# Kernel optimization log

Measured on AMD Instinct MI355X. Metric: run time of the kernel, lower is better.

Reference implementation:

```python
import jax, jax.numpy as jnp
import numpy as np
from jax import lax

D_MODEL, D_INNER, D_STATE, D_CONV, DT_RANK = 1024, 2048, 16, 4, 64
B_SZ, L = 2, 2048


def silu(v):
    return v * jax.nn.sigmoid(v)


def setup_inputs() -> dict:
    key = jax.random.key(0)
    ks = jax.random.split(key, 9)
    s = 0.02
    x = jax.random.normal(ks[0], (B_SZ, L, D_MODEL), jnp.float32)
    W_in = jax.random.normal(ks[1], (D_MODEL, 2 * D_INNER), jnp.float32) * s
    conv_w = jax.random.normal(ks[2], (D_INNER, D_CONV), jnp.float32) * 0.1  # depthwise kernel
    conv_b = jax.random.normal(ks[3], (D_INNER,), jnp.float32) * 0.01
    W_xproj = jax.random.normal(ks[4], (D_INNER, DT_RANK + 2 * D_STATE), jnp.float32) * s
    W_dt = jax.random.normal(ks[5], (DT_RANK, D_INNER), jnp.float32) * s
    b_dt = jax.random.normal(ks[6], (D_INNER,), jnp.float32) * 0.01
    A_log = jnp.log(jnp.tile(jnp.arange(1, D_STATE + 1, dtype=jnp.float32), (D_INNER, 1)))
    D = jnp.ones((D_INNER,), jnp.float32)
    W_out = jax.random.normal(ks[7], (D_INNER, D_MODEL), jnp.float32) * s
    return dict(x=x, W_in=W_in, conv_w=conv_w, conv_b=conv_b, W_xproj=W_xproj,
                W_dt=W_dt, b_dt=b_dt, A_log=A_log, D=D, W_out=W_out)


def reference(x, W_in, conv_w, conv_b, W_xproj, W_dt, b_dt, A_log, D, W_out):
    # in_proj, split into conv path u and gate res
    xr = x @ W_in                                  # (B, L, 2*d_inner)
    u, res = jnp.split(xr, 2, axis=-1)
    # causal depthwise conv1d (left-pad d_conv-1), then SiLU
    uc = jnp.swapaxes(u, 1, 2)                     # (B, C, L)
    uc = lax.conv_general_dilated(
        uc, conv_w[:, None, :], window_strides=(1,),
        padding=[(D_CONV - 1, 0)], feature_group_count=D_INNER,
        dimension_numbers=('NCH', 'OIH', 'NCH'))
    uc = uc + conv_b[None, :, None]
    u = silu(jnp.swapaxes(uc, 1, 2))               # (B, L, d_inner)
    # S6 projections
    x_dbl = u @ W_xproj                            # (B, L, dt_rank + 2*N)
    dt_low = x_dbl[..., :DT_RANK]
    Bm = x_dbl[..., DT_RANK:DT_RANK + D_STATE]     # (B, L, N)
    Cm = x_dbl[..., DT_RANK + D_STATE:]            # (B, L, N)
    dt = jax.nn.softplus(dt_low @ W_dt + b_dt)     # (B, L, d_inner)
    A = -jnp.exp(A_log)                            # (d_inner, N)
    # selective scan over time
    def step(h, inp):
        dt_t, B_t, C_t, u_t = inp                  # (B,d), (B,N), (B,N), (B,d)
        dA = jnp.exp(dt_t[:, :, None] * A)         # (B, d, N)
        dBu = dt_t[:, :, None] * B_t[:, None, :] * u_t[:, :, None]
        h = dA * h + dBu
        y = jnp.sum(h * C_t[:, None, :], axis=-1)  # (B, d)
        return h, y
    h0 = jnp.zeros((B_SZ, D_INNER, D_STATE), u.dtype)
    xs = (jnp.swapaxes(dt, 0, 1), jnp.swapaxes(Bm, 0, 1),
          jnp.swapaxes(Cm, 0, 1), jnp.swapaxes(u, 0, 1))
    _, ys = lax.scan(step, h0, xs)
    y = jnp.swapaxes(ys, 0, 1) + u * D             # (B, L, d_inner)
    # gate and out_proj
    y = y * silu(res)
    return y @ W_out
```

## Files before the change

### kernel.cpp

```cpp
#include <hip/hip_runtime.h>
#include <cstdint>
#include <cstddef>

#define DMODEL 1024
#define DINNER 2048
#define DSTATE 16
#define DCONV  4
#define DTRANK 64
#define BSZ    2
#define SEQL   2048
#define MROWS  (BSZ*SEQL)
#define NCHUNK 32
#define CLEN   (SEQL/NCHUNK)

typedef __bf16 bf16;
typedef bf16  bf16x8 __attribute__((ext_vector_type(8)));
typedef bf16  bf16x4 __attribute__((ext_vector_type(4)));
typedef float floatx4 __attribute__((ext_vector_type(4)));

#define EPILDC 136
#define SLDC   64

__device__ __forceinline__ float fsigmoid(float x){ return 1.f/(1.f+__expf(-x)); }
__device__ __forceinline__ float fsilu(float x){ return x*fsigmoid(x); }

__device__ __forceinline__ void gload_lds16(const void* g, void* l){
  __builtin_amdgcn_global_load_lds((__attribute__((address_space(1))) void*)g,
                                   (__attribute__((address_space(3))) void*)l,
                                   16, 0, 0);
}

__global__ void k_prep(const float* __restrict__ x, bf16* __restrict__ xb,
                       const float* __restrict__ W_in, const float* __restrict__ W_out,
                       const float* __restrict__ W_xproj, const float* __restrict__ W_dt,
                       bf16* __restrict__ WinT, bf16* __restrict__ WoutT,
                       bf16* __restrict__ WxT, bf16* __restrict__ WdtT){
  __shared__ float tile[32][33];
  int b = blockIdx.x;
  if (b < 4096){
    int i = (b*256 + threadIdx.x)*4;
    float4 v = *(const float4*)(x + i);
    bf16x4 o; o[0]=(bf16)v.x; o[1]=(bf16)v.y; o[2]=(bf16)v.z; o[3]=(bf16)v.w;
    *(bf16x4*)(xb + i) = o;
    return;
  }
  b -= 4096;
  const float* in; bf16* out; int R, C, outR, nbx;
  if      (b < 4096)            { in=W_in;    out=WinT;  R=1024; C=4096; outR=4096; nbx=128; }
  else if (b < 4096+2048)       { b-=4096;    in=W_out;  out=WoutT; R=2048; C=1024; outR=1024; nbx=32; }
  else if (b < 4096+2048+256)   { b-=6144;    in=W_xproj;out=WxT;  R=2048; C=96;   outR=128;  nbx=4; }
  else                          { b-=6400;    in=W_dt;   out=WdtT; R=64;   C=2048; outR=2048; nbx=64; }
  int c0 = (b % nbx)*32, r0 = (b / nbx)*32;
  int tx = threadIdx.x & 31, ty = threadIdx.x >> 5;
  #pragma unroll
  for (int ii=0; ii<4; ++ii){
    int r = r0 + ty + ii*8, c = c0 + tx;
    float v = 0.f;
    if (r < R && c < C) v = in[(size_t)r*C + c];
    tile[ty+ii*8][tx] = v;
  }
  __syncthreads();
  #pragma unroll
  for (int ii=0; ii<4; ++ii){
    int orow = c0 + ty + ii*8;
    int ocol = r0 + tx;
    if (orow < outR && ocol < R) out[(size_t)orow*R + ocol] = (bf16)tile[tx][ty+ii*8];
  }
}

__global__ __launch_bounds__(512, 2)
void k_gemm_in256(const bf16* __restrict__ A, const bf16* __restrict__ Bt,
                  bf16* __restrict__ C1, bf16* __restrict__ C2){
  extern __shared__ __align__(16) bf16 lds[];
  const int tid  = threadIdx.x;
  const int lane = tid & 63;
  const int wave = tid >> 6;
  const int quad = lane >> 4;
  const int mrow = lane & 15;
  const int wr = wave >> 2, wc = wave & 3;
  const int bm = blockIdx.y * 256, bn = blockIdx.x * 256;

  floatx4 acc[8][4];
  #pragma unroll
  for (int i=0;i<8;++i)
    #pragma unroll
    for (int j=0;j<4;++j) acc[i][j] = (floatx4){0.f,0.f,0.f,0.f};

  auto stage_tile = [&](int kt, int p){
    #pragma unroll
    for (int mat=0; mat<2; ++mat){
      const bf16* G = mat ? Bt : A;
      const int gb  = mat ? bn : bm;
      bf16* dst = lds + mat*32768 + p*16384 + tid*8;
      #pragma unroll
      for (int l=0; l<4; ++l){
        int L  = l*512 + tid;
        int rl = L >> 3;
        int cg = (L & 7) ^ (rl & 7);
        gload_lds16(G + (size_t)(gb + rl)*1024 + kt*64 + cg*8, dst + l*4096);
      }
    }
  };

  stage_tile(0, 0);

  for (int kt = 0; kt < 16; ++kt){
    const int p = kt & 1;
    if (kt < 15){
      stage_tile(kt+1, p^1);
      asm volatile("s_waitcnt vmcnt(8)" ::: "memory");
    } else {
      asm volatile("s_waitcnt vmcnt(0)" ::: "memory");
    }
    asm volatile("s_barrier" ::: "memory");
    const bf16* bA = lds + p*16384;
    const bf16* bB = lds + 32768 + p*16384;
    #pragma unroll
    for (int kk=0; kk<2; ++kk){
      bf16x8 bfr[4];
      #pragma unroll
      for (int j=0;j<4;++j){
        int r = wc*64 + j*16 + mrow;
        bfr[j] = *(const bf16x8*)(bB + r*64 + ((((kk<<2)|quad) ^ (r&7))*8));
      }
      #pragma unroll
      for (int mh=0; mh<2; ++mh){
        bf16x8 af[4];
        #pragma unroll
        for (int i=0;i<4;++i){
          int r = wr*128 + mh*64 + i*16 + mrow;
          af[i] = *(const bf16x8*)(bA + r*64 + ((((kk<<2)|quad) ^ (r&7))*8));
        }
        __builtin_amdgcn_s_setprio(1);
        #pragma unroll
        for (int i=0;i<4;++i)
          #pragma unroll
          for (int j=0;j<4;++j)
            acc[mh*4+i][j] = __builtin_amdgcn_mfma_f32_16x16x32_bf16(af[i], bfr[j], acc[mh*4+i][j], 0,0,0);
        __builtin_amdgcn_s_setprio(0);
      }
    }
    asm volatile("s_barrier" ::: "memory");
  }

  const bool isres = (bn >= DINNER);
  bf16* dst0 = isres ? (C2 + (bn - DINNER)) : (C1 + bn);
  #pragma unroll
  for (int h=0; h<2; ++h){
    asm volatile("s_barrier" ::: "memory");
    if (wr == h){
      #pragma unroll
      for (int a=0;a<8;++a){
        #pragma unroll
        for (int r=0;r<4;++r){
          int lrow = (a>>2)*64 + (a&3)*16 + quad*4 + r;
          #pragma unroll
          for (int j=0;j<4;++j){
            int lcol = wc*64 + j*16 + mrow;
            float v = acc[a][j][r];
            lds[lrow*264 + lcol] = (bf16)(isres ? fsilu(v) : v);
          }
        }
      }
    }
    asm volatile("s_barrier" ::: "memory");
    {
      int rr = tid >> 2, seg = (tid & 3)*64;
      bf16* gy = dst0 + (size_t)(bm + h*128 + rr)*DINNER + seg;
      #pragma unroll
      for (int i=0;i<8;++i)
        *(bf16x8*)(gy + i*8) = *(const bf16x8*)(lds + rr*264 + seg + i*8);
    }
  }
}

template<int EPI>
__global__ __launch_bounds__(256)
void k_gemm_bt(const bf16* __restrict__ A, const bf16* __restrict__ Bt,
               int M, int N, int K,
               float* __restrict__ C0, bf16* __restrict__ C1, bf16* __restrict__ C2,
               const float* __restrict__ bias){
  __shared__ bf16 lds[17408];
  const int tid  = threadIdx.x;
  const int lane = tid & 63;
  const int wave = tid >> 6;
  const int quad = lane >> 4;
  const int mrow = lane & 15;
  const int wr = wave >> 1, wc = wave & 1;
  const int bm = blockIdx.y * 128, bn = blockIdx.x * 128;
  const int Ks   = K / gridDim.z;
  const int kbeg = blockIdx.z * Ks;

  floatx4 acc[4][4];
  #pragma unroll
  for (int i=0;i<4;++i)
    #pragma unroll
    for (int j=0;j<4;++j) acc[i][j] = (floatx4){0.f,0.f,0.f,0.f};

  const int ar0 = tid >> 2;
  const int kc  = ((tid & 3) ^ ((ar0 >> 1) & 3)) * 8;
  const bf16* Ag0 = A  + (size_t)(bm + ar0)      * K + kc;
  const bf16* Ag1 = A  + (size_t)(bm + ar0 + 64) * K + kc;
  const bf16* Bg0 = Bt + (size_t)(bn + ar0)      * K + kc;
  const bf16* Bg1 = Bt + (size_t)(bn + ar0 + 64) * K + kc;
  const int ksl = (mrow >> 1) & 3;

  auto stage = [&](int k0, int p){
    bf16* bA = lds + p*4096;
    bf16* bB = lds + 8192 + p*4096;
    gload_lds16(Ag0 + k0, bA + (size_t)tid*8);
    gload_lds16(Ag1 + k0, bA + (size_t)(256+tid)*8);
    gload_lds16(Bg0 + k0, bB + (size_t)tid*8);
    gload_lds16(Bg1 + k0, bB + (size_t)(256+tid)*8);
  };

  stage(kbeg, 0);
  int p = 0;
  for (int k0 = kbeg; k0 < kbeg + Ks; k0 += 32){
    __syncthreads();
    if (k0 + 32 < kbeg + Ks) stage(k0 + 32, p ^ 1);
    const bf16* bA = lds + p*4096;
    const bf16* bB = lds + 8192 + p*4096;
    bf16x8 af[4], bfr[4];
    #pragma unroll
    for (int i=0;i<4;++i)
      af[i] = *(const bf16x8*)(bA + (wr*64 + i*16 + mrow)*32 + (quad ^ ksl)*8);
    #pragma unroll
    for (int j=0;j<4;++j)
      bfr[j] = *(const bf16x8*)(bB + (wc*64 + j*16 + mrow)*32 + (quad ^ ksl)*8);
    #pragma unroll
    for (int i=0;i<4;++i)
      #pragma unroll
      for (int j=0;j<4;++j)
        acc[i][j] = __builtin_amdgcn_mfma_f32_16x16x32_bf16(af[i], bfr[j], acc[i][j], 0,0,0);
    p ^= 1;
  }

  if (EPI == 0){
    float* Cz = C0 + (size_t)blockIdx.z * M * N;
    #pragma unroll
    for (int i=0;i<4;++i){
      #pragma unroll
      for (int r=0;r<4;++r){
        int row = bm + wr*64 + i*16 + quad*4 + r;
        #pragma unroll
        for (int j=0;j<4;++j){
          int col = bn + wc*64 + j*16 + mrow;
          Cz[(size_t)row*N + col] = acc[i][j][r];
        }
      }
    }
  } else {
    __syncthreads();
    const bool isres = (bn >= DINNER);
    #pragma unroll
    for (int i=0;i<4;++i)
      #pragma unroll
      for (int r=0;r<4;++r){
        int lrow = wr*64 + i*16 + quad*4 + r;
        #pragma unroll
        for (int j=0;j<4;++j){
          int lcol = wc*64 + j*16 + mrow;
          float v = acc[i][j][r];
          lds[lrow*EPILDC + lcol] = (bf16)(isres ? fsilu(v) : v);
        }
      }
    __syncthreads();
    bf16* dst = isres ? (C2 + (bn - DINNER)) : (C1 + bn);
    const int rr = tid >> 1, hh = (tid & 1)*64;
    #pragma unroll
    for (int i=0;i<8;++i)
      *(bf16x8*)(dst + (size_t)(bm + rr)*DINNER + hh + i*8) =
        *(const bf16x8*)(lds + rr*EPILDC + hh + i*8);
  }
}

__global__ void k_xdbl_reduce(const float* __restrict__ part, float* __restrict__ xdbl,
                              bf16* __restrict__ dtlowb){
  int t = blockIdx.x*blockDim.x + threadIdx.x;
  int i4 = t*4;
  floatx4 acc = (floatx4){0.f,0.f,0.f,0.f};
  #pragma unroll
  for (int z=0; z<8; ++z)
    acc += *(const floatx4*)(part + (size_t)z*MROWS*128 + i4);
  *(floatx4*)(xdbl + i4) = acc;
  int r = i4 >> 7, c = i4 & 127;
  if (c < DTRANK){
    bf16x4 o; o[0]=(bf16)acc[0]; o[1]=(bf16)acc[1]; o[2]=(bf16)acc[2]; o[3]=(bf16)acc[3];
    *(bf16x4*)(dtlowb + (size_t)r*DTRANK + c) = o;
  }
}

__global__ void k_out_reduce(const float* __restrict__ part, float* __restrict__ out){
  int i4 = (blockIdx.x*blockDim.x + threadIdx.x)*4;
  floatx4 a = *(const floatx4*)(part + i4);
  floatx4 b = *(const floatx4*)(part + (size_t)MROWS*DMODEL + i4);
  *(floatx4*)(out + i4) = a + b;
}

__global__ void k_conv_silu(const bf16* __restrict__ u_pre,
                            const float* __restrict__ conv_w,
                            const float* __restrict__ conv_b,
                            bf16* __restrict__ ub){
  int t   = blockIdx.x*blockDim.x + threadIdx.x;
  int d4  = (t & (DINNER/4-1))*4;
  int row = t >> 9;
  int l   = row & (SEQL-1);
  float4 cb = *(const float4*)(conv_b + d4);
  float acc[4] = {cb.x, cb.y, cb.z, cb.w};
  float4 w0 = *(const float4*)(conv_w + (d4+0)*4);
  float4 w1 = *(const float4*)(conv_w + (d4+1)*4);
  float4 w2 = *(const float4*)(conv_w + (d4+2)*4);
  float4 w3 = *(const float4*)(conv_w + (d4+3)*4);
  float wk[4][4] = {{w0.x,w0.y,w0.z,w0.w},{w1.x,w1.y,w1.z,w1.w},
                    {w2.x,w2.y,w2.z,w2.w},{w3.x,w3.y,w3.z,w3.w}};
  #pragma unroll
  for (int k=0;k<4;++k){
    int lk = l + k - 3;
    if (lk >= 0){
      bf16x4 uv = *(const bf16x4*)(u_pre + (size_t)(row + k - 3)*DINNER + d4);
      #pragma unroll
      for (int j=0;j<4;++j) acc[j] += (float)uv[j] * wk[j][k];
    }
  }
  bf16x4 o;
  #pragma unroll
  for (int j=0;j<4;++j) o[j] = (bf16)fsilu(acc[j]);
  *(bf16x4*)(ub + (size_t)row*DINNER + d4) = o;
}

__device__ __forceinline__ void dt_tile_stage(const bf16* __restrict__ dtlow,
                                              const bf16* __restrict__ WdtT,
                                              int base_row, int d0, int tid,
                                              bf16* sdt, bf16* swdt){
  int r  = tid >> 2;
  int c2 = (tid & 3)*2, sw = r & 7;
  const bf16* gA = dtlow + (size_t)(base_row + r)*DTRANK + c2*8;
  const bf16* gB = WdtT  + (size_t)(d0 + r)*DTRANK + c2*8;
  *(bf16x8*)(sdt  + r*64 + ((c2  )^sw)*8) = *(const bf16x8*)(gA);
  *(bf16x8*)(sdt  + r*64 + ((c2+1)^sw)*8) = *(const bf16x8*)(gA + 8);
  *(bf16x8*)(swdt + r*64 + ((c2  )^sw)*8) = *(const bf16x8*)(gB);
  *(bf16x8*)(swdt + r*64 + ((c2+1)^sw)*8) = *(const bf16x8*)(gB + 8);
}

__device__ __forceinline__ void dt_tile_compute(const float* __restrict__ b_dt,
                                                int d0, int tid,
                                                bf16* sdt, const bf16* swdt){
  int wave = tid >> 6, lane = tid & 63;
  int quad = lane >> 4, mrow = lane & 15;
  int arow = wave*16 + mrow;
  bf16x8 af0 = *(const bf16x8*)(sdt + arow*64 + ((quad    ) ^ (arow&7))*8);
  bf16x8 af1 = *(const bf16x8*)(sdt + arow*64 + ((quad + 4) ^ (arow&7))*8);
  #pragma unroll
  for (int dj=0; dj<4; ++dj){
    int brow = dj*16 + mrow;
    bf16x8 bf0 = *(const bf16x8*)(swdt + brow*64 + ((quad    ) ^ (brow&7))*8);
    bf16x8 bf1 = *(const bf16x8*)(swdt + brow*64 + ((quad + 4) ^ (brow&7))*8);
    floatx4 a = (floatx4){0.f,0.f,0.f,0.f};
    a = __builtin_amdgcn_mfma_f32_16x16x32_bf16(af0, bf0, a, 0,0,0);
    a = __builtin_amdgcn_mfma_f32_16x16x32_bf16(af1, bf1, a, 0,0,0);
    float bias = b_dt[d0 + dj*16 + mrow];
    #pragma unroll
    for (int rr=0; rr<4; ++rr){
      float z = a[rr] + bias;
      float sp = fmaxf(z, 0.f) + __logf(1.f + __expf(-fabsf(z)));
      sdt[(wave*16 + quad*4 + rr)*64 + dj*16 + mrow] = (bf16)sp;
    }
  }
}

__global__ void k_scan_phase1(const bf16* __restrict__ dtlow, const bf16* __restrict__ WdtT,
                              const float* __restrict__ b_dt,
                              const bf16* __restrict__ ub,
                              const float* __restrict__ x_dbl, const float* __restrict__ A_log,
                              float* __restrict__ Pbuf, float* __restrict__ Sbuf){
  __shared__ bf16 sdt[64*64], sub[64*SLDC], swdt[64*64];
  __shared__ float sB[64*16];
  const int tid = threadIdx.x;
  int t  = blockIdx.x*256 + tid;
  int g  = t & 3;
  int d  = (t >> 2) & (DINNER-1);
  int dloc = d & 63, d0 = d & ~63;
  int bc = t >> 13;
  int c  = bc & (NCHUNK-1);
  int b  = bc >> 5;
  int base_row = b*SEQL + c*CLEN;
  {
    int r = tid >> 2, ch = (tid & 3)*16;
    const bf16* gu = ub + (size_t)(base_row + r)*DINNER + d0 + ch;
    *(bf16x8*)(sub + r*SLDC + ch)     = *(const bf16x8*)(gu);
    *(bf16x8*)(sub + r*SLDC + ch + 8) = *(const bf16x8*)(gu + 8);
    int q = tid & 3;
    *(floatx4*)(sB + r*16 + q*4) =
      *(const floatx4*)(x_dbl + (size_t)(base_row + r)*128 + DTRANK + q*4);
    dt_tile_stage(dtlow, WdtT, base_row, d0, tid, sdt, swdt);
  }
  floatx4 alog = *(const floatx4*)(A_log + d*DSTATE + g*4);
  float an[4];
  #pragma unroll
  for (int n=0;n<4;++n) an[n] = -__expf(alog[n]);
  __syncthreads();
  dt_tile_compute(b_dt, d0, tid, sdt, swdt);
  __syncthreads();
  float sumdt = 0.f, S[4] = {0.f,0.f,0.f,0.f};
  #pragma unroll 8
  for (int s=0; s<CLEN; ++s){
    float dtv = (float)sdt[s*SLDC + dloc];
    float du  = dtv * (float)sub[s*SLDC + dloc];
    floatx4 Bv = *(const floatx4*)(sB + s*16 + g*4);
    sumdt += dtv;
    #pragma unroll
    for (int n=0;n<4;++n){
      float e = __expf(dtv*an[n]);
      S[n]  = fmaf(S[n], e, du*Bv[n]);
    }
  }
  size_t ob = ((size_t)bc*DINNER + d)*DSTATE + g*4;
  floatx4 Pv, Sv = {S[0],S[1],S[2],S[3]};
  #pragma unroll
  for (int n=0;n<4;++n) Pv[n] = __expf(an[n]*sumdt);
  *(floatx4*)(Pbuf + ob) = Pv;
  *(floatx4*)(Sbuf + ob) = Sv;
}

__global__ void k_scan_phase2(const float* __restrict__ Pbuf, float* __restrict__ Sbuf){
  int t = blockIdx.x*blockDim.x + threadIdx.x;
  int b   = t >> 15;
  int rem = t & 32767;
  float h = 0.f;
  for (int c=0;c<NCHUNK;++c){
    size_t ix = (size_t)(b*NCHUNK + c)*DINNER*DSTATE + rem;
    float p = Pbuf[ix], s = Sbuf[ix];
    Sbuf[ix] = h;
    h = fmaf(p, h, s);
  }
}

__global__ void k_scan_phase3(const bf16* __restrict__ dtlow, const bf16* __restrict__ WdtT,
                              const float* __restrict__ b_dt,
                              const bf16* __restrict__ ub,
                              const float* __restrict__ x_dbl, const float* __restrict__ A_log,
                              const float* __restrict__ Dvec, const float* __restrict__ Hin,
                              const bf16* __restrict__ resb, bf16* __restrict__ yb){
  __shared__ bf16 sdt[64*64], sub[64*SLDC], srs[64*SLDC], swdt[64*64];
  __shared__ float sBC[64*32];
  bf16* syb = swdt;
  const int tid = threadIdx.x;
  int t  = blockIdx.x*256 + tid;
  int g  = t & 3;
  int d  = (t >> 2) & (DINNER-1);
  int dloc = d & 63, d0 = d & ~63;
  int bc = t >> 13;
  int c  = bc & (NCHUNK-1);
  int b  = bc >> 5;
  int base_row = b*SEQL + c*CLEN;
  {
    int r = tid >> 2, ch = (tid & 3)*16;
    const bf16* gu = ub   + (size_t)(base_row + r)*DINNER + d0 + ch;
    const bf16* gr = resb + (size_t)(base_row + r)*DINNER + d0 + ch;
    *(bf16x8*)(sub + r*SLDC + ch)     = *(const bf16x8*)(gu);
    *(bf16x8*)(sub + r*SLDC + ch + 8) = *(const bf16x8*)(gu + 8);
    *(bf16x8*)(srs + r*SLDC + ch)     = *(const bf16x8*)(gr);
    *(bf16x8*)(srs + r*SLDC + ch + 8) = *(const bf16x8*)(gr + 8);
    int q = tid & 3;
    const float* gx = x_dbl + (size_t)(base_row + r)*128 + DTRANK;
    *(floatx4*)(sBC + r*32 + q*4)      = *(const floatx4*)(gx + q*4);
    *(floatx4*)(sBC + r*32 + 16 + q*4) = *(const floatx4*)(gx + DSTATE + q*4);
    dt_tile_stage(dtlow, WdtT, base_row, d0, tid, sdt, swdt);
  }
  floatx4 alog = *(const floatx4*)(A_log + d*DSTATE + g*4);
  float an[4];
  #pragma unroll
  for (int n=0;n<4;++n) an[n] = -__expf(alog[n]);
  floatx4 h = *(const floatx4*)(Hin + ((size_t)bc*DINNER + d)*DSTATE + g*4);
  float Dd = Dvec[d];
  __syncthreads();
  dt_tile_compute(b_dt, d0, tid, sdt, swdt);
  __syncthreads();
  #pragma unroll 8
  for (int s=0; s<CLEN; ++s){
    float dtv = (float)sdt[s*SLDC + dloc];
    float uv  = (float)sub[s*SLDC + dloc];
    float du  = dtv*uv;
    floatx4 Bv = *(const floatx4*)(sBC + s*32 + g*4);
    floatx4 Cv = *(const floatx4*)(sBC + s*32 + 16 + g*4);
    float y = 0.f;
    #pragma unroll
    for (int n=0;n<4;++n){
      float e = __expf(dtv*an[n]);
      h[n] = fmaf(h[n], e, du*Bv[n]);
      y = fmaf(h[n], Cv[n], y);
    }
    y += __shfl_xor(y, 1);
    y += __shfl_xor(y, 2);
    if (g == 0){
      y = (y + uv*Dd) * (float)srs[s*SLDC + dloc];
      syb[s*64 + dloc] = (bf16)y;
    }
  }
  __syncthreads();
  {
    int r = tid >> 2, ch = (tid & 3)*16;
    bf16* gy = yb + (size_t)(base_row + r)*DINNER + d0 + ch;
    *(bf16x8*)(gy)     = *(const bf16x8*)(syb + r*64 + ch);
    *(bf16x8*)(gy + 8) = *(const bf16x8*)(syb + r*64 + ch + 8);
  }
}

extern "C" void kernel_launch(void* const* d_in, const int* in_sizes, int n_in,
                              void* d_out, int out_size, void* d_ws, size_t ws_size,
                              hipStream_t stream){
  const float* x      = (const float*)d_in[0];
  const float* W_in   = (const float*)d_in[1];
  const float* conv_w = (const float*)d_in[2];
  const float* conv_b = (const float*)d_in[3];
  const float* W_xproj= (const float*)d_in[4];
  const float* W_dt   = (const float*)d_in[5];
  const float* b_dt   = (const float*)d_in[6];
  const float* A_log  = (const float*)d_in[7];
  const float* Dv     = (const float*)d_in[8];
  const float* W_out  = (const float*)d_in[9];
  float* out = (float*)d_out;

  uint8_t* wp = (uint8_t*)d_ws;
  auto alloc = [&](size_t bytes)->void*{ void* p = wp; wp += (bytes + 255) & ~(size_t)255; return p; };
  bf16*  xb     = (bf16*) alloc((size_t)MROWS*DMODEL*2);
  bf16*  WinT   = (bf16*) alloc((size_t)2*DINNER*DMODEL*2);
  bf16*  WoutT  = (bf16*) alloc((size_t)DMODEL*DINNER*2);
  bf16*  WxT    = (bf16*) alloc((size_t)128*DINNER*2);
  bf16*  WdtT   = (bf16*) alloc((size_t)DINNER*DTRANK*2);
  bf16*  updt   = (bf16*) alloc((size_t)MROWS*DINNER*2);
  float* scanPS = (float*)alloc((size_t)2*BSZ*NCHUNK*DSTATE*DINNER*4);
  float* Pbuf   = scanPS;
  float* Sbuf   = scanPS + (size_t)BSZ*NCHUNK*DSTATE*DINNER;
  float* xdbl_part = scanPS;
  float* outpart   = (float*)updt;
  bf16*  resb   = (bf16*) alloc((size_t)MROWS*DINNER*2);
  bf16*  ub     = (bf16*) alloc((size_t)MROWS*DINNER*2);
  float* xdbl   = (float*)alloc((size_t)MROWS*128*4);
  bf16*  dtlowb = (bf16*) alloc((size_t)MROWS*DTRANK*2);
  bf16*  yb     = (bf16*) alloc((size_t)MROWS*DINNER*2);

  static bool lds_attr_set = false;
  if (!lds_attr_set){
    hipFuncSetAttribute((const void*)k_gemm_in256,
                        hipFuncAttributeMaxDynamicSharedMemorySize, 131072);
    lds_attr_set = true;
  }

  k_prep<<<4096 + 4096+2048+256+128, 256, 0, stream>>>(x, xb, W_in, W_out, W_xproj, W_dt,
                                                       WinT, WoutT, WxT, WdtT);

  k_gemm_in256<<<dim3(4096/256, 4096/256), 512, 131072, stream>>>(xb, WinT, updt, resb);
  k_conv_silu<<<MROWS*DINNER/4/256, 256, 0, stream>>>(updt, conv_w, conv_b, ub);
  k_gemm_bt<0><<<dim3(1, 4096/128, 8), 256, 0, stream>>>(ub, WxT, MROWS, 128, DINNER, xdbl_part, nullptr, nullptr, nullptr);
  k_xdbl_reduce<<<(MROWS*128/4)/256, 256, 0, stream>>>(xdbl_part, xdbl, dtlowb);
  k_scan_phase1<<<BSZ*NCHUNK*DINNER*4/256, 256, 0, stream>>>(dtlowb, WdtT, b_dt, ub, xdbl, A_log, Pbuf, Sbuf);
  k_scan_phase2<<<BSZ*DINNER*DSTATE/256, 256, 0, stream>>>(Pbuf, Sbuf);
  k_scan_phase3<<<BSZ*NCHUNK*DINNER*4/256, 256, 0, stream>>>(dtlowb, WdtT, b_dt, ub, xdbl, A_log, Dv, Sbuf, resb, yb);
  k_gemm_bt<0><<<dim3(1024/128, 4096/128, 2), 256, 0, stream>>>(yb, WoutT, MROWS, DMODEL, DINNER, outpart, nullptr, nullptr, nullptr);
  k_out_reduce<<<(MROWS*DMODEL/4)/256, 256, 0, stream>>>(outpart, out);
}
```

Before: 309.8 us.

## Interleave in-proj GEMM loads with MFMA phases; drop split-K on out-proj

The 256x256 in-projection GEMM now issues the next tile's A and B loads separately and interleaves them with four barrier-separated MFMA phases, so global-to-LDS copies overlap compute in finer steps. The out-projection GEMM no longer uses 2-way split-K plus a separate reduce kernel. It writes fp32 output directly through a new LDS-staged epilogue with coalesced vector stores. The trade-off is many more barriers per k-step in the big GEMM, and half as many blocks (256) for the output GEMM.

Measured after the change: 317.5 us. 1.02x slower.

```diff
diff --git a/kernel.cpp b/kernel.cpp
--- a/kernel.cpp
+++ b/kernel.cpp
@@ -86,60 +86,91 @@
     #pragma unroll
     for (int j=0;j<4;++j) acc[i][j] = (floatx4){0.f,0.f,0.f,0.f};
 
-  auto stage_tile = [&](int kt, int p){
-    #pragma unroll
-    for (int mat=0; mat<2; ++mat){
-      const bf16* G = mat ? Bt : A;
-      const int gb  = mat ? bn : bm;
-      bf16* dst = lds + mat*32768 + p*16384 + tid*8;
-      #pragma unroll
-      for (int l=0; l<4; ++l){
-        int L  = l*512 + tid;
-        int rl = L >> 3;
-        int cg = (L & 7) ^ (rl & 7);
-        gload_lds16(G + (size_t)(gb + rl)*1024 + kt*64 + cg*8, dst + l*4096);
-      }
+  auto issue_mat = [&](int kt, int p, int mat){
+    const bf16* G = mat ? Bt : A;
+    const int gb  = mat ? bn : bm;
+    bf16* dst = lds + mat*32768 + p*16384 + tid*8;
+    #pragma unroll
+    for (int l=0; l<4; ++l){
+      int L  = l*512 + tid;
+      int rl = L >> 3;
+      int cg = (L & 7) ^ (rl & 7);
+      gload_lds16(G + (size_t)(gb + rl)*1024 + kt*64 + cg*8, dst + l*4096);
     }
   };
 
-  stage_tile(0, 0);
+  auto read_af = [&](const bf16* bA, int mh, int kk, bf16x8* af){
+    #pragma unroll
+    for (int i=0;i<4;++i){
+      int r = wr*128 + mh*64 + i*16 + mrow;
+      af[i] = *(const bf16x8*)(bA + r*64 + ((((kk<<2)|quad) ^ (r&7))*8));
+    }
+  };
+  auto read_bf = [&](const bf16* bB, int kk, bf16x8* bfr){
+    #pragma unroll
+    for (int j=0;j<4;++j){
+      int r = wc*64 + j*16 + mrow;
+      bfr[j] = *(const bf16x8*)(bB + r*64 + ((((kk<<2)|quad) ^ (r&7))*8));
+    }
+  };
+
+  issue_mat(0,0,0); issue_mat(0,0,1);
 
   for (int kt = 0; kt < 16; ++kt){
     const int p = kt & 1;
+    const bf16* bA = lds + p*16384;
+    const bf16* bB = lds + 32768 + p*16384;
+    bf16x8 af[4], bfr[4];
+
     if (kt < 15){
-      stage_tile(kt+1, p^1);
-      asm volatile("s_waitcnt vmcnt(8)" ::: "memory");
+      issue_mat(kt+1, p^1, 0);
+      asm volatile("s_waitcnt vmcnt(4)" ::: "memory");
     } else {
       asm volatile("s_waitcnt vmcnt(0)" ::: "memory");
     }
     asm volatile("s_barrier" ::: "memory");
-    const bf16* bA = lds + p*16384;
-    const bf16* bB = lds + 32768 + p*16384;
-    #pragma unroll
-    for (int kk=0; kk<2; ++kk){
-      bf16x8 bfr[4];
-      #pragma unroll
-      for (int j=0;j<4;++j){
-        int r = wc*64 + j*16 + mrow;
-        bfr[j] = *(const bf16x8*)(bB + r*64 + ((((kk<<2)|quad) ^ (r&7))*8));
-      }
-      #pragma unroll
-      for (int mh=0; mh<2; ++mh){
-        bf16x8 af[4];
-        #pragma unroll
-        for (int i=0;i<4;++i){
-          int r = wr*128 + mh*64 + i*16 + mrow;
-          af[i] = *(const bf16x8*)(bA + r*64 + ((((kk<<2)|quad) ^ (r&7))*8));
-        }
-        __builtin_amdgcn_s_setprio(1);
-        #pragma unroll
-        for (int i=0;i<4;++i)
-          #pragma unroll
-          for (int j=0;j<4;++j)
-            acc[mh*4+i][j] = __builtin_amdgcn_mfma_f32_16x16x32_bf16(af[i], bfr[j], acc[mh*4+i][j], 0,0,0);
-        __builtin_amdgcn_s_setprio(0);
-      }
-    }
+    read_af(bA, 0, 0, af); read_bf(bB, 0, bfr);
+    __builtin_amdgcn_s_setprio(1);
+    #pragma unroll
+    for (int i=0;i<4;++i)
+      #pragma unroll
+      for (int j=0;j<4;++j)
+        acc[i][j] = __builtin_amdgcn_mfma_f32_16x16x32_bf16(af[i], bfr[j], acc[i][j], 0,0,0);
+    __builtin_amdgcn_s_setprio(0);
+    asm volatile("s_barrier" ::: "memory");
+
+    if (kt < 15) issue_mat(kt+1, p^1, 1);
+    read_af(bA, 1, 0, af);
+    asm volatile("s_barrier" ::: "memory");
+    __builtin_amdgcn_s_setprio(1);
+    #pragma unroll
+    for (int i=0;i<4;++i)
+      #pragma unroll
+      for (int j=0;j<4;++j)
+        acc[4+i][j] = __builtin_amdgcn_mfma_f32_16x16x32_bf16(af[i], bfr[j], acc[4+i][j], 0,0,0);
+    __builtin_amdgcn_s_setprio(0);
+    asm volatile("s_barrier" ::: "memory");
+
+    read_af(bA, 0, 1, af); read_bf(bB, 1, bfr);
+    asm volatile("s_barrier" ::: "memory");
+    __builtin_amdgcn_s_setprio(1);
+    #pragma unroll
+    for (int i=0;i<4;++i)
+      #pragma unroll
+      for (int j=0;j<4;++j)
+        acc[i][j] = __builtin_amdgcn_mfma_f32_16x16x32_bf16(af[i], bfr[j], acc[i][j], 0,0,0);
+    __builtin_amdgcn_s_setprio(0);
+    asm volatile("s_barrier" ::: "memory");
+
+    read_af(bA, 1, 1, af);
+    asm volatile("s_barrier" ::: "memory");
+    __builtin_amdgcn_s_setprio(1);
+    #pragma unroll
+    for (int i=0;i<4;++i)
+      #pragma unroll
+      for (int j=0;j<4;++j)
+        acc[4+i][j] = __builtin_amdgcn_mfma_f32_16x16x32_bf16(af[i], bfr[j], acc[4+i][j], 0,0,0);
+    __builtin_amdgcn_s_setprio(0);
     asm volatile("s_barrier" ::: "memory");
   }
 
@@ -180,7 +211,7 @@
                int M, int N, int K,
                float* __restrict__ C0, bf16* __restrict__ C1, bf16* __restrict__ C2,
                const float* __restrict__ bias){
-  __shared__ bf16 lds[17408];
+  __shared__ __align__(16) bf16 lds[17408];
   const int tid  = threadIdx.x;
   const int lane = tid & 63;
   const int wave = tid >> 6;
@@ -250,7 +281,7 @@
         }
       }
     }
-  } else {
+  } else if (EPI == 1){
     __syncthreads();
     const bool isres = (bn >= DINNER);
     #pragma unroll
@@ -272,6 +303,31 @@
     for (int i=0;i<8;++i)
       *(bf16x8*)(dst + (size_t)(bm + rr)*DINNER + hh + i*8) =
         *(const bf16x8*)(lds + rr*EPILDC + hh + i*8);
+  } else {
+    float* lf = (float*)lds;
+    #pragma unroll
+    for (int h=0; h<2; ++h){
+      __syncthreads();
+      if (wr == h){
+        #pragma unroll
+        for (int i=0;i<4;++i)
+          #pragma unroll
+          for (int r=0;r<4;++r){
+            int lrow = i*16 + quad*4 + r;
+            #pragma unroll
+            for (int j=0;j<4;++j)
+              lf[lrow*132 + wc*64 + j*16 + mrow] = acc[i][j][r];
+          }
+      }
+      __syncthreads();
+      {
+        int rr = tid >> 2, seg = tid & 3;
+        float* gy = C0 + (size_t)(bm + h*64 + rr)*N + bn + seg*32;
+        #pragma unroll
+        for (int i=0;i<8;++i)
+          *(floatx4*)(gy + i*4) = *(const floatx4*)(lf + rr*132 + seg*32 + i*4);
+      }
+    }
   }
 }
 
@@ -289,13 +345,6 @@
     bf16x4 o; o[0]=(bf16)acc[0]; o[1]=(bf16)acc[1]; o[2]=(bf16)acc[2]; o[3]=(bf16)acc[3];
     *(bf16x4*)(dtlowb + (size_t)r*DTRANK + c) = o;
   }
-}
-
-__global__ void k_out_reduce(const float* __restrict__ part, float* __restrict__ out){
-  int i4 = (blockIdx.x*blockDim.x + threadIdx.x)*4;
-  floatx4 a = *(const floatx4*)(part + i4);
-  floatx4 b = *(const floatx4*)(part + (size_t)MROWS*DMODEL + i4);
-  *(floatx4*)(out + i4) = a + b;
 }
 
 __global__ void k_conv_silu(const bf16* __restrict__ u_pre,
@@ -534,7 +583,6 @@
   float* Pbuf   = scanPS;
   float* Sbuf   = scanPS + (size_t)BSZ*NCHUNK*DSTATE*DINNER;
   float* xdbl_part = scanPS;
-  float* outpart   = (float*)updt;
   bf16*  resb   = (bf16*) alloc((size_t)MROWS*DINNER*2);
   bf16*  ub     = (bf16*) alloc((size_t)MROWS*DINNER*2);
   float* xdbl   = (float*)alloc((size_t)MROWS*128*4);
@@ -558,6 +606,5 @@
   k_scan_phase1<<<BSZ*NCHUNK*DINNER*4/256, 256, 0, stream>>>(dtlowb, WdtT, b_dt, ub, xdbl, A_log, Pbuf, Sbuf);
   k_scan_phase2<<<BSZ*DINNER*DSTATE/256, 256, 0, stream>>>(Pbuf, Sbuf);
   k_scan_phase3<<<BSZ*NCHUNK*DINNER*4/256, 256, 0, stream>>>(dtlowb, WdtT, b_dt, ub, xdbl, A_log, Dv, Sbuf, resb, yb);
-  k_gemm_bt<0><<<dim3(1024/128, 4096/128, 2), 256, 0, stream>>>(yb, WoutT, MROWS, DMODEL, DINNER, outpart, nullptr, nullptr, nullptr);
-  k_out_reduce<<<(MROWS*DMODEL/4)/256, 256, 0, stream>>>(outpart, out);
-}
+  k_gemm_bt<2><<<dim3(1024/128, 4096/128), 256, 0, stream>>>(yb, WoutT, MROWS, DMODEL, DINNER, out, nullptr, nullptr, nullptr);
+}
```
